# Optimization experiments

Measured on AMD Instinct MI355X. Metric: run time of the kernel, lower is better.

Reference implementation:

```python
import jax, jax.numpy as jnp
import numpy as np

N_FEAT = 64      # number of continuous features
N_BINS = 255     # bin edges per feature (EBM default) -> 256 score slots incl. OOV
N_PAIRS = 32     # interaction terms
BATCH = 262144


def _bin_indices(edges, x):
    """TF Discretization (searchsorted right) + IntegerLookup(vocab=range(B), OOV->0).
    edges: [N, B] sorted per row; x: [batch, N] -> int32 [batch, N] in [0, B]."""
    idx = jax.vmap(lambda e, col: jnp.searchsorted(e, col, side='right'),
                   in_axes=(0, 1), out_axes=1)(edges, x)  # [batch, N], values 0..B
    B = edges.shape[1]
    # IntegerLookup: value v in {0..B-1} -> v+1 ; value B (not in vocab) -> OOV index 0
    return jnp.where(idx < B, idx + 1, 0)


def setup_inputs() -> dict:
    key = jax.random.key(0)
    ks = jax.random.split(key, 6)
    x = jax.random.normal(ks[0], (BATCH, N_FEAT), dtype=jnp.float32)
    edges = jnp.sort(jax.random.normal(ks[1], (N_FEAT, N_BINS), dtype=jnp.float32), axis=1)
    pair_edges = jnp.sort(jax.random.normal(ks[2], (N_FEAT, N_BINS), dtype=jnp.float32), axis=1)
    w = jax.random.normal(ks[3], (N_FEAT, N_BINS + 1), dtype=jnp.float32) * 0.1
    tables = jax.random.normal(ks[4], (N_PAIRS, N_BINS + 1, N_BINS + 1), dtype=jnp.float32) * 0.1
    pairs = jax.random.randint(ks[5], (N_PAIRS, 2), 0, N_FEAT, dtype=jnp.int32)
    bias = jnp.zeros((1,), dtype=jnp.float32)
    return {"x": x, "edges": edges, "w": w, "pair_edges": pair_edges,
            "pairs": pairs, "tables": tables, "bias": bias}


def reference(x, edges, w, pair_edges, pairs, tables, bias):
    # --- per-feature main effects: one_hot(idx) @ Dense(1) == gather w[f, idx] ---
    idx = _bin_indices(edges, x)                                  # [batch, N]
    feat = w[jnp.arange(N_FEAT)[None, :], idx]                    # [batch, N]
    # --- pairwise interactions: gather_nd on [L, R] lookup tables ---
    pidx = _bin_indices(pair_edges, x)                            # [batch, N]
    li = pidx[:, pairs[:, 0]]                                     # [batch, P]
    ri = pidx[:, pairs[:, 1]]                                     # [batch, P]
    inter = tables[jnp.arange(N_PAIRS)[None, :], li, ri]          # [batch, P]
    # --- BiasLayer: reduce_sum(concat, axis=1) + bias, then sigmoid ---
    logits = jnp.sum(feat, axis=1) + jnp.sum(inter, axis=1) + bias[0]
    return jax.nn.sigmoid(logits)                                  # [batch]
```

## Files before the change

kernel.cpp:

```cpp
#include <hip/hip_runtime.h>
#include <hip/hip_fp16.h>

#define NBINS 255
#define NPAIRS 32
#define BIGF 3.0e38f


__global__ void ebm_prep(const float* __restrict__ edges,
                         const float* __restrict__ pair_edges,
                         const float* __restrict__ w,
                         float* __restrict__ ws) {
    int tid = blockIdx.x * blockDim.x + threadIdx.x;
    int f = tid >> 8, j = tid & 255;
    float* E  = ws;
    float* PE = ws + 16384;
    float* ME = ws + 32768;
    float* MP = ws + 36864;
    float* CU = ws + 40960;
    float* CP = ws + 41984;
    __half* W = (__half*)(ws + 43008);
    E[tid]  = (j < NBINS) ? edges[f * NBINS + j]      : BIGF;
    PE[tid] = (j < NBINS) ? pair_edges[f * NBINS + j] : BIGF;
    int src = (j < 255) ? j + 1 : 0;
    W[tid]  = __float2half(w[f * 256 + src]);
    if (j < 64) {
        int idx = 4 * j + 3;
        ME[f * 64 + j] = (idx < NBINS) ? edges[f * NBINS + idx]      : BIGF;
        MP[f * 64 + j] = (idx < NBINS) ? pair_edges[f * NBINS + idx] : BIGF;
    }
    if (j < 16) {
        CU[f * 16 + j] = (j < 15) ? edges[f * NBINS + 16 * j + 15]      : BIGF;
        CP[f * 16 + j] = (j < 15) ? pair_edges[f * NBINS + 16 * j + 15] : BIGF;
    }
}

__global__ void ebm_prep_tables(const float* __restrict__ tables,
                                unsigned short* __restrict__ o) {
    int i = blockIdx.x * blockDim.x + threadIdx.x;
    int b = i & 255, a = (i >> 8) & 255, p = i >> 16;
    int ra = (a < 255) ? a + 1 : 0;
    int rb = (b < 255) ? b + 1 : 0;
    o[i] = __half_as_ushort(__float2half(tables[(p << 16) + (ra << 8) + rb]));
}

__device__ __forceinline__ unsigned pick16(const unsigned* pw, int s) {
    unsigned v01 = (s & 1) ? pw[1]  : pw[0];
    unsigned v23 = (s & 1) ? pw[3]  : pw[2];
    unsigned v45 = (s & 1) ? pw[5]  : pw[4];
    unsigned v67 = (s & 1) ? pw[7]  : pw[6];
    unsigned v89 = (s & 1) ? pw[9]  : pw[8];
    unsigned vab = (s & 1) ? pw[11] : pw[10];
    unsigned vcd = (s & 1) ? pw[13] : pw[12];
    unsigned vef = (s & 1) ? pw[15] : pw[14];
    unsigned w0 = (s & 2) ? v23 : v01;
    unsigned w1 = (s & 2) ? v67 : v45;
    unsigned w2 = (s & 2) ? vab : v89;
    unsigned w3 = (s & 2) ? vef : vcd;
    unsigned u0 = (s & 4) ? w1 : w0;
    unsigned u1 = (s & 4) ? w3 : w2;
    return (s & 8) ? u1 : u0;
}

__global__ __launch_bounds__(1024) void ebm_main(
    const float* __restrict__ x,
    const int*   __restrict__ pairs,
    const float* __restrict__ tables_f32,
    const float* __restrict__ bias,
    const float* __restrict__ ws,
    const __half* __restrict__ T16,
    int useT16,
    float*       __restrict__ out) {

    __shared__ float  sE[16384];
    __shared__ float  sPE[16384];
    __shared__ float4 sME[1024];
    __shared__ float4 sMP[1024];

    int tid = threadIdx.x;
    {
        const float4* w4 = (const float4*)ws;
        float4* dE = (float4*)sE;
        float4* dP = (float4*)sPE;
        for (int i = tid; i < 4096; i += 1024) {
            dE[i] = w4[i];
            dP[i] = w4[4096 + i];
        }
        if (tid < 1024) {
            sME[tid] = w4[8192 + tid];
            sMP[tid] = w4[9216 + tid];
        }
    }
    const float*  CU = ws + 40960;
    const float*  CP = ws + 41984;
    const __half* Wg = (const __half*)(ws + 43008);
    float bias0 = bias[0];

    __syncthreads();

    int row = blockIdx.x * 1024 + tid;
    const float4* x4 = (const float4*)x + row * 16;
    const float4* sE4 = (const float4*)sE;
    const float4* sP4 = (const float4*)sPE;

    float acc = 0.f;
    unsigned pw[16];

    float4 xg = x4[0];
#pragma unroll
    for (int g = 0; g < 16; ++g) {
        float4 xnext = xg;
        if (g < 15) xnext = x4[g + 1];
        float xf[4] = {xg.x, xg.y, xg.z, xg.w};

        int t[4];
#pragma unroll
        for (int j = 0; j < 4; ++j) {
            const float* cu = CU + (4 * g + j) * 16;
            int tt = 0;
#pragma unroll
            for (int k = 0; k < 15; ++k) tt += (xf[j] >= cu[k]);
            t[j] = tt;
        }
        int t2[4];
#pragma unroll
        for (int j = 0; j < 4; ++j) {
            const float* cp = CP + (4 * g + j) * 16;
            int tt = 0;
#pragma unroll
            for (int k = 0; k < 15; ++k) tt += (xf[j] >= cp[k]);
            t2[j] = tt;
        }
        float4 mu[4], mp[4];
#pragma unroll
        for (int j = 0; j < 4; ++j) mu[j] = sME[(4 * g + j) * 16 + t[j]];
#pragma unroll
        for (int j = 0; j < 4; ++j) mp[j] = sMP[(4 * g + j) * 16 + t2[j]];
        int lo[4], lo2[4];
        float4 fu[4], fp[4];
#pragma unroll
        for (int j = 0; j < 4; ++j) {
            int m = (xf[j] >= mu[j].x) + (xf[j] >= mu[j].y) + (xf[j] >= mu[j].z);
            lo[j] = 4 * t[j] + m;
            fu[j] = sE4[(4 * g + j) * 64 + lo[j]];
        }
#pragma unroll
        for (int j = 0; j < 4; ++j) {
            int m = (xf[j] >= mp[j].x) + (xf[j] >= mp[j].y) + (xf[j] >= mp[j].z);
            lo2[j] = 4 * t2[j] + m;
            fp[j] = sP4[(4 * g + j) * 64 + lo2[j]];
        }
#pragma unroll
        for (int j = 0; j < 4; ++j) {
            int c = 4 * lo[j] + (xf[j] >= fu[j].x) + (xf[j] >= fu[j].y) +
                    (xf[j] >= fu[j].z) + (xf[j] >= fu[j].w);
            acc += __half2float(Wg[(4 * g + j) * 256 + c]);
        }
        unsigned pword = 0;
#pragma unroll
        for (int j = 0; j < 4; ++j) {
            int c2 = 4 * lo2[j] + (xf[j] >= fp[j].x) + (xf[j] >= fp[j].y) +
                     (xf[j] >= fp[j].z) + (xf[j] >= fp[j].w);
            pword |= (unsigned)c2 << (8 * j);
        }
        pw[g] = pword;
        xg = xnext;
    }

    if (useT16) {
#pragma unroll
        for (int p = 0; p < NPAIRS; ++p) {
            int a = pairs[2 * p], b = pairs[2 * p + 1];
            unsigned wa = pick16(pw, a >> 2);
            unsigned wb = pick16(pw, b >> 2);
            int li = (wa >> ((a & 3) * 8)) & 255;
            int ri = (wb >> ((b & 3) * 8)) & 255;
            acc += __half2float(T16[(p << 16) + (li << 8) + ri]);
        }
    } else {
#pragma unroll
        for (int p = 0; p < NPAIRS; ++p) {
            int a = pairs[2 * p], b = pairs[2 * p + 1];
            unsigned wa = pick16(pw, a >> 2);
            unsigned wb = pick16(pw, b >> 2);
            int li = (wa >> ((a & 3) * 8)) & 255;
            int ri = (wb >> ((b & 3) * 8)) & 255;
            int lb = (li < 255) ? li + 1 : 0;
            int rb = (ri < 255) ? ri + 1 : 0;
            acc += tables_f32[(p << 16) + (lb << 8) + rb];
        }
    }

    out[row] = 1.0f / (1.0f + __expf(-(acc + bias0)));
}

extern "C" void kernel_launch(void* const* d_in, const int* in_sizes, int n_in,
                              void* d_out, int out_size, void* d_ws, size_t ws_size,
                              hipStream_t stream) {
    const float* x          = (const float*)d_in[0];
    const float* edges      = (const float*)d_in[1];
    const float* w          = (const float*)d_in[2];
    const float* pair_edges = (const float*)d_in[3];
    const int*   pairs      = (const int*)d_in[4];
    const float* tables     = (const float*)d_in[5];
    const float* bias       = (const float*)d_in[6];
    float* out = (float*)d_out;
    float* ws  = (float*)d_ws;

    int useT16 = (ws_size >= (size_t)4399104) ? 1 : 0;
    __half* T16 = (__half*)((char*)d_ws + 204800);

    ebm_prep<<<64, 256, 0, stream>>>(edges, pair_edges, w, ws);
    if (useT16) {
        ebm_prep_tables<<<2048, 1024, 0, stream>>>(tables, (unsigned short*)T16);
    }
    ebm_main<<<256, 1024, 0, stream>>>(x, pairs, tables, bias, ws, T16, useT16, out);
}
```

Before: 193.5 us.

## Split each row across two wavefront halves and halve shared memory footprint

Each block now handles 512 rows with two threads per row. Each half bins 32 features and handles 16 of the pair lookups, with the bin codes exchanged through shared memory and the partial sums combined before the sigmoid. Pair-edge arrays are read from global memory instead of being staged in LDS, which cuts LDS per block roughly in half so more blocks can be resident, and the grid doubles. This costs extra barriers, an LDS exchange step, and uncached-in-LDS global reads for the pair edges.

```diff
diff --git a/kernel.cpp b/kernel.cpp
--- a/kernel.cpp
+++ b/kernel.cpp
@@ -61,7 +61,7 @@
     return (s & 8) ? u1 : u0;
 }
 
-__global__ __launch_bounds__(1024) void ebm_main(
+__global__ __launch_bounds__(1024, 8) void ebm_main(
     const float* __restrict__ x,
     const int*   __restrict__ pairs,
     const float* __restrict__ tables_f32,
@@ -72,50 +72,49 @@
     float*       __restrict__ out) {
 
     __shared__ float  sE[16384];
-    __shared__ float  sPE[16384];
     __shared__ float4 sME[1024];
-    __shared__ float4 sMP[1024];
 
     int tid = threadIdx.x;
     {
         const float4* w4 = (const float4*)ws;
         float4* dE = (float4*)sE;
-        float4* dP = (float4*)sPE;
-        for (int i = tid; i < 4096; i += 1024) {
-            dE[i] = w4[i];
-            dP[i] = w4[4096 + i];
-        }
-        if (tid < 1024) {
-            sME[tid] = w4[8192 + tid];
-            sMP[tid] = w4[9216 + tid];
-        }
-    }
-    const float*  CU = ws + 40960;
-    const float*  CP = ws + 41984;
-    const __half* Wg = (const __half*)(ws + 43008);
+        for (int i = tid; i < 4096; i += 1024) dE[i] = w4[i];
+        sME[tid] = w4[8192 + tid];
+    }
+    const float*  CU  = ws + 40960;
+    const float*  CP  = ws + 41984;
+    const __half* Wg  = (const __half*)(ws + 43008);
+    const float4* PE4 = (const float4*)(ws + 16384);
+    const float4* MP4 = (const float4*)(ws + 36864);
     float bias0 = bias[0];
 
     __syncthreads();
 
-    int row = blockIdx.x * 1024 + tid;
-    const float4* x4 = (const float4*)x + row * 16;
+    int wv   = tid >> 6;
+    int lane = tid & 63;
+    int half = wv >> 3;
+    int halfU = __builtin_amdgcn_readfirstlane(half);
+    int rowl = (wv & 7) * 64 + lane;
+    int row  = blockIdx.x * 512 + rowl;
+
+    const float4* x4  = (const float4*)x + row * 16 + halfU * 8;
     const float4* sE4 = (const float4*)sE;
-    const float4* sP4 = (const float4*)sPE;
 
     float acc = 0.f;
-    unsigned pw[16];
+    unsigned pw[8];
 
     float4 xg = x4[0];
 #pragma unroll
-    for (int g = 0; g < 16; ++g) {
+    for (int g = 0; g < 8; ++g) {
+        int fb = (halfU * 8 + g) * 4;
         float4 xnext = xg;
-        if (g < 15) xnext = x4[g + 1];
+        if (g < 7) xnext = x4[g + 1];
         float xf[4] = {xg.x, xg.y, xg.z, xg.w};
 
         int t[4];
 #pragma unroll
         for (int j = 0; j < 4; ++j) {
-            const float* cu = CU + (4 * g + j) * 16;
+            const float* cu = CU + (fb + j) * 16;
             int tt = 0;
 #pragma unroll
             for (int k = 0; k < 15; ++k) tt += (xf[j] >= cu[k]);
@@ -124,7 +123,7 @@
         int t2[4];
 #pragma unroll
         for (int j = 0; j < 4; ++j) {
-            const float* cp = CP + (4 * g + j) * 16;
+            const float* cp = CP + (fb + j) * 16;
             int tt = 0;
 #pragma unroll
             for (int k = 0; k < 15; ++k) tt += (xf[j] >= cp[k]);
@@ -132,28 +131,28 @@
         }
         float4 mu[4], mp[4];
 #pragma unroll
-        for (int j = 0; j < 4; ++j) mu[j] = sME[(4 * g + j) * 16 + t[j]];
-#pragma unroll
-        for (int j = 0; j < 4; ++j) mp[j] = sMP[(4 * g + j) * 16 + t2[j]];
+        for (int j = 0; j < 4; ++j) mu[j] = sME[(fb + j) * 16 + t[j]];
+#pragma unroll
+        for (int j = 0; j < 4; ++j) mp[j] = MP4[(fb + j) * 16 + t2[j]];
         int lo[4], lo2[4];
         float4 fu[4], fp[4];
 #pragma unroll
         for (int j = 0; j < 4; ++j) {
             int m = (xf[j] >= mu[j].x) + (xf[j] >= mu[j].y) + (xf[j] >= mu[j].z);
             lo[j] = 4 * t[j] + m;
-            fu[j] = sE4[(4 * g + j) * 64 + lo[j]];
+            fu[j] = sE4[(fb + j) * 64 + lo[j]];
         }
 #pragma unroll
         for (int j = 0; j < 4; ++j) {
             int m = (xf[j] >= mp[j].x) + (xf[j] >= mp[j].y) + (xf[j] >= mp[j].z);
             lo2[j] = 4 * t2[j] + m;
-            fp[j] = sP4[(4 * g + j) * 64 + lo2[j]];
+            fp[j] = PE4[(fb + j) * 64 + lo2[j]];
         }
 #pragma unroll
         for (int j = 0; j < 4; ++j) {
             int c = 4 * lo[j] + (xf[j] >= fu[j].x) + (xf[j] >= fu[j].y) +
                     (xf[j] >= fu[j].z) + (xf[j] >= fu[j].w);
-            acc += __half2float(Wg[(4 * g + j) * 256 + c]);
+            acc += __half2float(Wg[(fb + j) * 256 + c]);
         }
         unsigned pword = 0;
 #pragma unroll
@@ -166,22 +165,43 @@
         xg = xnext;
     }
 
+    unsigned* scr  = (unsigned*)sE;
+    float*    accS = (float*)sME;
+    __syncthreads();
+#pragma unroll
+    for (int i = 0; i < 8; ++i)
+        scr[(i * 2 + halfU) * 512 + rowl] = pw[i];
+    __syncthreads();
+    unsigned oth[8];
+#pragma unroll
+    for (int i = 0; i < 8; ++i)
+        oth[i] = scr[(i * 2 + (1 - halfU)) * 512 + rowl];
+    unsigned pwAll[16];
+#pragma unroll
+    for (int i = 0; i < 8; ++i) {
+        pwAll[i]     = halfU ? oth[i] : pw[i];
+        pwAll[8 + i] = halfU ? pw[i]  : oth[i];
+    }
+
+    int pbase = halfU * 16;
     if (useT16) {
 #pragma unroll
-        for (int p = 0; p < NPAIRS; ++p) {
+        for (int q = 0; q < 16; ++q) {
+            int p = pbase + q;
             int a = pairs[2 * p], b = pairs[2 * p + 1];
-            unsigned wa = pick16(pw, a >> 2);
-            unsigned wb = pick16(pw, b >> 2);
+            unsigned wa = pick16(pwAll, a >> 2);
+            unsigned wb = pick16(pwAll, b >> 2);
             int li = (wa >> ((a & 3) * 8)) & 255;
             int ri = (wb >> ((b & 3) * 8)) & 255;
             acc += __half2float(T16[(p << 16) + (li << 8) + ri]);
         }
     } else {
 #pragma unroll
-        for (int p = 0; p < NPAIRS; ++p) {
+        for (int q = 0; q < 16; ++q) {
+            int p = pbase + q;
             int a = pairs[2 * p], b = pairs[2 * p + 1];
-            unsigned wa = pick16(pw, a >> 2);
-            unsigned wb = pick16(pw, b >> 2);
+            unsigned wa = pick16(pwAll, a >> 2);
+            unsigned wb = pick16(pwAll, b >> 2);
             int li = (wa >> ((a & 3) * 8)) & 255;
             int ri = (wb >> ((b & 3) * 8)) & 255;
             int lb = (li < 255) ? li + 1 : 0;
@@ -190,7 +210,12 @@
         }
     }
 
-    out[row] = 1.0f / (1.0f + __expf(-(acc + bias0)));
+    accS[halfU * 512 + rowl] = acc;
+    __syncthreads();
+    if (halfU == 0) {
+        float tot = acc + accS[512 + rowl];
+        out[row] = 1.0f / (1.0f + __expf(-(tot + bias0)));
+    }
 }
 
 extern "C" void kernel_launch(void* const* d_in, const int* in_sizes, int n_in,
@@ -213,5 +238,5 @@
     if (useT16) {
         ebm_prep_tables<<<2048, 1024, 0, stream>>>(tables, (unsigned short*)T16);
     }
-    ebm_main<<<256, 1024, 0, stream>>>(x, pairs, tables, bias, ws, T16, useT16, out);
-}
+    ebm_main<<<512, 1024, 0, stream>>>(x, pairs, tables, bias, ws, T16, useT16, out);
+}
```

Result: slower. 207.0 us (+7.0%).

## Software-pipeline bin search across feature groups and index pair bytes via LDS

Applied to the files above, without the earlier changes.

Restructures the main loop so the coarse search and first-level LDS lookups for the next feature group run while the current group finishes, and the weight gathers are deferred one iteration. The register select tree (pick16) for pair indices is replaced by staging the packed bin bytes in reused shared memory and reading them with byte loads. Pair feature ids are broadcast from one wave register with readlane instead of scalar loads. This raises register pressure and adds a barrier plus LDS stores, and it sets a launch-bounds occupancy hint.

```diff
diff --git a/kernel.cpp b/kernel.cpp
--- a/kernel.cpp
+++ b/kernel.cpp
@@ -43,25 +43,7 @@
     o[i] = __half_as_ushort(__float2half(tables[(p << 16) + (ra << 8) + rb]));
 }
 
-__device__ __forceinline__ unsigned pick16(const unsigned* pw, int s) {
-    unsigned v01 = (s & 1) ? pw[1]  : pw[0];
-    unsigned v23 = (s & 1) ? pw[3]  : pw[2];
-    unsigned v45 = (s & 1) ? pw[5]  : pw[4];
-    unsigned v67 = (s & 1) ? pw[7]  : pw[6];
-    unsigned v89 = (s & 1) ? pw[9]  : pw[8];
-    unsigned vab = (s & 1) ? pw[11] : pw[10];
-    unsigned vcd = (s & 1) ? pw[13] : pw[12];
-    unsigned vef = (s & 1) ? pw[15] : pw[14];
-    unsigned w0 = (s & 2) ? v23 : v01;
-    unsigned w1 = (s & 2) ? v67 : v45;
-    unsigned w2 = (s & 2) ? vab : v89;
-    unsigned w3 = (s & 2) ? vef : vcd;
-    unsigned u0 = (s & 4) ? w1 : w0;
-    unsigned u1 = (s & 4) ? w3 : w2;
-    return (s & 8) ? u1 : u0;
-}
-
-__global__ __launch_bounds__(1024) void ebm_main(
+__global__ __launch_bounds__(1024, 4) void ebm_main(
     const float* __restrict__ x,
     const int*   __restrict__ pairs,
     const float* __restrict__ tables_f32,
@@ -77,6 +59,7 @@
     __shared__ float4 sMP[1024];
 
     int tid = threadIdx.x;
+    int myab = pairs[tid & 63];
     {
         const float4* w4 = (const float4*)ws;
         float4* dE = (float4*)sE;
@@ -85,10 +68,8 @@
             dE[i] = w4[i];
             dP[i] = w4[4096 + i];
         }
-        if (tid < 1024) {
-            sME[tid] = w4[8192 + tid];
-            sMP[tid] = w4[9216 + tid];
-        }
+        sME[tid] = w4[8192 + tid];
+        sMP[tid] = w4[9216 + tid];
     }
     const float*  CU = ws + 40960;
     const float*  CP = ws + 41984;
@@ -98,62 +79,94 @@
     __syncthreads();
 
     int row = blockIdx.x * 1024 + tid;
-    const float4* x4 = (const float4*)x + row * 16;
+    const float4* x4  = (const float4*)x + row * 16;
     const float4* sE4 = (const float4*)sE;
     const float4* sP4 = (const float4*)sPE;
 
     float acc = 0.f;
     unsigned pw[16];
 
-    float4 xg = x4[0];
+    float4 xa = x4[0];
+    float4 xb = x4[1];
+    float xf[4] = {xa.x, xa.y, xa.z, xa.w};
+    int t[4], t2[4];
+#pragma unroll
+    for (int j = 0; j < 4; ++j) {
+        const float* cu = CU + j * 16;
+        int tt = 0;
+#pragma unroll
+        for (int k = 0; k < 15; ++k) tt += (xf[j] >= cu[k]);
+        t[j] = tt;
+    }
+#pragma unroll
+    for (int j = 0; j < 4; ++j) {
+        const float* cp = CP + j * 16;
+        int tt = 0;
+#pragma unroll
+        for (int k = 0; k < 15; ++k) tt += (xf[j] >= cp[k]);
+        t2[j] = tt;
+    }
+    float4 mu[4], mp[4];
+#pragma unroll
+    for (int j = 0; j < 4; ++j) mu[j] = sME[j * 16 + t[j]];
+#pragma unroll
+    for (int j = 0; j < 4; ++j) mp[j] = sMP[j * 16 + t2[j]];
+
+    __half wraw[4];
+#pragma unroll
+    for (int j = 0; j < 4; ++j) wraw[j] = __float2half(0.f);
+
 #pragma unroll
     for (int g = 0; g < 16; ++g) {
-        float4 xnext = xg;
-        if (g < 15) xnext = x4[g + 1];
-        float xf[4] = {xg.x, xg.y, xg.z, xg.w};
-
-        int t[4];
-#pragma unroll
-        for (int j = 0; j < 4; ++j) {
-            const float* cu = CU + (4 * g + j) * 16;
-            int tt = 0;
-#pragma unroll
-            for (int k = 0; k < 15; ++k) tt += (xf[j] >= cu[k]);
-            t[j] = tt;
-        }
-        int t2[4];
-#pragma unroll
-        for (int j = 0; j < 4; ++j) {
-            const float* cp = CP + (4 * g + j) * 16;
-            int tt = 0;
-#pragma unroll
-            for (int k = 0; k < 15; ++k) tt += (xf[j] >= cp[k]);
-            t2[j] = tt;
-        }
-        float4 mu[4], mp[4];
-#pragma unroll
-        for (int j = 0; j < 4; ++j) mu[j] = sME[(4 * g + j) * 16 + t[j]];
-#pragma unroll
-        for (int j = 0; j < 4; ++j) mp[j] = sMP[(4 * g + j) * 16 + t2[j]];
+        int fb = 4 * g;
         int lo[4], lo2[4];
         float4 fu[4], fp[4];
 #pragma unroll
         for (int j = 0; j < 4; ++j) {
             int m = (xf[j] >= mu[j].x) + (xf[j] >= mu[j].y) + (xf[j] >= mu[j].z);
             lo[j] = 4 * t[j] + m;
-            fu[j] = sE4[(4 * g + j) * 64 + lo[j]];
+            fu[j] = sE4[(fb + j) * 64 + lo[j]];
         }
 #pragma unroll
         for (int j = 0; j < 4; ++j) {
             int m = (xf[j] >= mp[j].x) + (xf[j] >= mp[j].y) + (xf[j] >= mp[j].z);
             lo2[j] = 4 * t2[j] + m;
-            fp[j] = sP4[(4 * g + j) * 64 + lo2[j]];
-        }
+            fp[j] = sP4[(fb + j) * 64 + lo2[j]];
+        }
+        float xfn[4] = {xb.x, xb.y, xb.z, xb.w};
+        int tn[4] = {0, 0, 0, 0}, t2n[4] = {0, 0, 0, 0};
+        if (g < 15) {
+#pragma unroll
+            for (int j = 0; j < 4; ++j) {
+                const float* cu = CU + (fb + 4 + j) * 16;
+                int tt = 0;
+#pragma unroll
+                for (int k = 0; k < 15; ++k) tt += (xfn[j] >= cu[k]);
+                tn[j] = tt;
+            }
+#pragma unroll
+            for (int j = 0; j < 4; ++j) {
+                const float* cp = CP + (fb + 4 + j) * 16;
+                int tt = 0;
+#pragma unroll
+                for (int k = 0; k < 15; ++k) tt += (xfn[j] >= cp[k]);
+                t2n[j] = tt;
+            }
+        }
+        float4 mun[4], mpn[4];
+        if (g < 15) {
+#pragma unroll
+            for (int j = 0; j < 4; ++j) mun[j] = sME[(fb + 4 + j) * 16 + tn[j]];
+#pragma unroll
+            for (int j = 0; j < 4; ++j) mpn[j] = sMP[(fb + 4 + j) * 16 + t2n[j]];
+        }
+#pragma unroll
+        for (int j = 0; j < 4; ++j) acc += __half2float(wraw[j]);
 #pragma unroll
         for (int j = 0; j < 4; ++j) {
             int c = 4 * lo[j] + (xf[j] >= fu[j].x) + (xf[j] >= fu[j].y) +
                     (xf[j] >= fu[j].z) + (xf[j] >= fu[j].w);
-            acc += __half2float(Wg[(4 * g + j) * 256 + c]);
+            wraw[j] = Wg[(fb + j) * 256 + c];
         }
         unsigned pword = 0;
 #pragma unroll
@@ -163,27 +176,42 @@
             pword |= (unsigned)c2 << (8 * j);
         }
         pw[g] = pword;
-        xg = xnext;
-    }
+        if (g < 15) {
+#pragma unroll
+            for (int j = 0; j < 4; ++j) {
+                xf[j] = xfn[j]; t[j] = tn[j]; t2[j] = t2n[j];
+                mu[j] = mun[j]; mp[j] = mpn[j];
+            }
+            xa = xb;
+            if (g < 14) xb = x4[g + 2];
+        }
+    }
+#pragma unroll
+    for (int j = 0; j < 4; ++j) acc += __half2float(wraw[j]);
+
+    __syncthreads();
+    unsigned* scr = (unsigned*)sE;
+#pragma unroll
+    for (int i = 0; i < 16; ++i) scr[i * 1024 + tid] = pw[i];
+    const unsigned char* scrB = (const unsigned char*)sE;
+    int boff = tid * 4;
 
     if (useT16) {
 #pragma unroll
         for (int p = 0; p < NPAIRS; ++p) {
-            int a = pairs[2 * p], b = pairs[2 * p + 1];
-            unsigned wa = pick16(pw, a >> 2);
-            unsigned wb = pick16(pw, b >> 2);
-            int li = (wa >> ((a & 3) * 8)) & 255;
-            int ri = (wb >> ((b & 3) * 8)) & 255;
+            int a = __builtin_amdgcn_readlane(myab, 2 * p);
+            int b = __builtin_amdgcn_readlane(myab, 2 * p + 1);
+            int li = scrB[(a >> 2) * 4096 + boff + (a & 3)];
+            int ri = scrB[(b >> 2) * 4096 + boff + (b & 3)];
             acc += __half2float(T16[(p << 16) + (li << 8) + ri]);
         }
     } else {
 #pragma unroll
         for (int p = 0; p < NPAIRS; ++p) {
-            int a = pairs[2 * p], b = pairs[2 * p + 1];
-            unsigned wa = pick16(pw, a >> 2);
-            unsigned wb = pick16(pw, b >> 2);
-            int li = (wa >> ((a & 3) * 8)) & 255;
-            int ri = (wb >> ((b & 3) * 8)) & 255;
+            int a = __builtin_amdgcn_readlane(myab, 2 * p);
+            int b = __builtin_amdgcn_readlane(myab, 2 * p + 1);
+            int li = scrB[(a >> 2) * 4096 + boff + (a & 3)];
+            int ri = scrB[(b >> 2) * 4096 + boff + (b & 3)];
             int lb = (li < 255) ? li + 1 : 0;
             int rb = (ri < 255) ? ri + 1 : 0;
             acc += tables_f32[(p << 16) + (lb << 8) + rb];
```

After: 200.7 us. 3.7% more time.

## Split main kernel into half-feature binning and separate pair-lookup kernels

Applied to the files above, without the earlier changes.

Replaces the single fused kernel with two kernels when workspace is large enough. The first bins each row using two blocks per 1024 rows, each handling half of the features with half the shared-memory edge tables, and writes partial logits and packed pair bins to global memory. The second kernel reads those back, does the 32 table lookups and applies the sigmoid. The aim is more blocks and less shared memory per block for better occupancy, paid for with extra global traffic (about 16 words per row) and one more launch. It only takes effect if the harness workspace exceeds the new size threshold.

```diff
diff --git a/kernel.cpp b/kernel.cpp
--- a/kernel.cpp
+++ b/kernel.cpp
@@ -43,6 +43,151 @@
     o[i] = __half_as_ushort(__float2half(tables[(p << 16) + (ra << 8) + rb]));
 }
 
+__global__ __launch_bounds__(1024, 8) void ebm_bin(
+    const float* __restrict__ x,
+    const float* __restrict__ ws,
+    float*       __restrict__ plog,
+    unsigned*    __restrict__ pbins) {
+
+    __shared__ float  sE[8192];
+    __shared__ float  sPE[8192];
+    __shared__ float4 sME[512];
+    __shared__ float4 sMP[512];
+
+    int tid = threadIdx.x;
+    int h = blockIdx.x & 1;
+    int rowbase = (blockIdx.x >> 1) * 1024;
+    {
+        const float4* w4 = (const float4*)ws;
+        float4* dE = (float4*)sE;
+        float4* dP = (float4*)sPE;
+        for (int i = tid; i < 2048; i += 1024) {
+            dE[i] = w4[h * 2048 + i];
+            dP[i] = w4[4096 + h * 2048 + i];
+        }
+        if (tid < 512) {
+            sME[tid] = w4[8192 + h * 512 + tid];
+            sMP[tid] = w4[9216 + h * 512 + tid];
+        }
+    }
+    const float*  CU = ws + 40960 + h * 512;
+    const float*  CP = ws + 41984 + h * 512;
+    const __half* Wg = (const __half*)(ws + 43008);
+
+    __syncthreads();
+
+    int row = rowbase + tid;
+    const float4* x4  = (const float4*)x + row * 16 + h * 8;
+    const float4* sE4 = (const float4*)sE;
+    const float4* sP4 = (const float4*)sPE;
+
+    float acc = 0.f;
+
+    float4 xg = x4[0];
+#pragma unroll
+    for (int g = 0; g < 8; ++g) {
+        int fb = 4 * g;
+        float4 xnext = xg;
+        if (g < 7) xnext = x4[g + 1];
+        float xf[4] = {xg.x, xg.y, xg.z, xg.w};
+
+        int t[4];
+#pragma unroll
+        for (int j = 0; j < 4; ++j) {
+            const float* cu = CU + (fb + j) * 16;
+            int tt = 0;
+#pragma unroll
+            for (int k = 0; k < 15; ++k) tt += (xf[j] >= cu[k]);
+            t[j] = tt;
+        }
+        int t2[4];
+#pragma unroll
+        for (int j = 0; j < 4; ++j) {
+            const float* cp = CP + (fb + j) * 16;
+            int tt = 0;
+#pragma unroll
+            for (int k = 0; k < 15; ++k) tt += (xf[j] >= cp[k]);
+            t2[j] = tt;
+        }
+        float4 mu[4], mp[4];
+#pragma unroll
+        for (int j = 0; j < 4; ++j) mu[j] = sME[(fb + j) * 16 + t[j]];
+#pragma unroll
+        for (int j = 0; j < 4; ++j) mp[j] = sMP[(fb + j) * 16 + t2[j]];
+        int lo[4], lo2[4];
+        float4 fu[4], fp[4];
+#pragma unroll
+        for (int j = 0; j < 4; ++j) {
+            int m = (xf[j] >= mu[j].x) + (xf[j] >= mu[j].y) + (xf[j] >= mu[j].z);
+            lo[j] = 4 * t[j] + m;
+            fu[j] = sE4[(fb + j) * 64 + lo[j]];
+        }
+#pragma unroll
+        for (int j = 0; j < 4; ++j) {
+            int m = (xf[j] >= mp[j].x) + (xf[j] >= mp[j].y) + (xf[j] >= mp[j].z);
+            lo2[j] = 4 * t2[j] + m;
+            fp[j] = sP4[(fb + j) * 64 + lo2[j]];
+        }
+#pragma unroll
+        for (int j = 0; j < 4; ++j) {
+            int c = 4 * lo[j] + (xf[j] >= fu[j].x) + (xf[j] >= fu[j].y) +
+                    (xf[j] >= fu[j].z) + (xf[j] >= fu[j].w);
+            acc += __half2float(Wg[(h * 32 + fb + j) * 256 + c]);
+        }
+        unsigned pword = 0;
+#pragma unroll
+        for (int j = 0; j < 4; ++j) {
+            int c2 = 4 * lo2[j] + (xf[j] >= fp[j].x) + (xf[j] >= fp[j].y) +
+                     (xf[j] >= fp[j].z) + (xf[j] >= fp[j].w);
+            pword |= (unsigned)c2 << (8 * j);
+        }
+        pbins[(h * 8 + g) * 262144 + row] = pword;
+        xg = xnext;
+    }
+
+    plog[h * 262144 + row] = acc;
+}
+
+__global__ __launch_bounds__(1024, 8) void ebm_pairs(
+    const int*      __restrict__ pairs,
+    const float*    __restrict__ tables_f32,
+    const float*    __restrict__ bias,
+    const float*    __restrict__ plog,
+    const unsigned* __restrict__ pbins,
+    const __half*   __restrict__ T16,
+    int useT16,
+    float*          __restrict__ out) {
+
+    int row = blockIdx.x * 1024 + threadIdx.x;
+    float acc = plog[row] + plog[262144 + row] + bias[0];
+
+    if (useT16) {
+#pragma unroll
+        for (int p = 0; p < NPAIRS; ++p) {
+            int a = pairs[2 * p], b = pairs[2 * p + 1];
+            unsigned wa = pbins[(a >> 2) * 262144 + row];
+            unsigned wb = pbins[(b >> 2) * 262144 + row];
+            int li = (wa >> ((a & 3) * 8)) & 255;
+            int ri = (wb >> ((b & 3) * 8)) & 255;
+            acc += __half2float(T16[(p << 16) + (li << 8) + ri]);
+        }
+    } else {
+#pragma unroll
+        for (int p = 0; p < NPAIRS; ++p) {
+            int a = pairs[2 * p], b = pairs[2 * p + 1];
+            unsigned wa = pbins[(a >> 2) * 262144 + row];
+            unsigned wb = pbins[(b >> 2) * 262144 + row];
+            int li = (wa >> ((a & 3) * 8)) & 255;
+            int ri = (wb >> ((b & 3) * 8)) & 255;
+            int lb = (li < 255) ? li + 1 : 0;
+            int rb = (ri < 255) ? ri + 1 : 0;
+            acc += tables_f32[(p << 16) + (lb << 8) + rb];
+        }
+    }
+
+    out[row] = 1.0f / (1.0f + __expf(-acc));
+}
+
 __device__ __forceinline__ unsigned pick16(const unsigned* pw, int s) {
     unsigned v01 = (s & 1) ? pw[1]  : pw[0];
     unsigned v23 = (s & 1) ? pw[3]  : pw[2];
@@ -61,7 +206,7 @@
     return (s & 8) ? u1 : u0;
 }
 
-__global__ __launch_bounds__(1024) void ebm_main(
+__global__ __launch_bounds__(1024, 4) void ebm_main_mono(
     const float* __restrict__ x,
     const int*   __restrict__ pairs,
     const float* __restrict__ tables_f32,
@@ -85,10 +230,8 @@
             dE[i] = w4[i];
             dP[i] = w4[4096 + i];
         }
-        if (tid < 1024) {
-            sME[tid] = w4[8192 + tid];
-            sMP[tid] = w4[9216 + tid];
-        }
+        sME[tid] = w4[8192 + tid];
+        sMP[tid] = w4[9216 + tid];
     }
     const float*  CU = ws + 40960;
     const float*  CP = ws + 41984;
@@ -98,7 +241,7 @@
     __syncthreads();
 
     int row = blockIdx.x * 1024 + tid;
-    const float4* x4 = (const float4*)x + row * 16;
+    const float4* x4  = (const float4*)x + row * 16;
     const float4* sE4 = (const float4*)sE;
     const float4* sP4 = (const float4*)sPE;
 
@@ -108,6 +251,7 @@
     float4 xg = x4[0];
 #pragma unroll
     for (int g = 0; g < 16; ++g) {
+        int fb = 4 * g;
         float4 xnext = xg;
         if (g < 15) xnext = x4[g + 1];
         float xf[4] = {xg.x, xg.y, xg.z, xg.w};
@@ -115,7 +259,7 @@
         int t[4];
 #pragma unroll
         for (int j = 0; j < 4; ++j) {
-            const float* cu = CU + (4 * g + j) * 16;
+            const float* cu = CU + (fb + j) * 16;
             int tt = 0;
 #pragma unroll
             for (int k = 0; k < 15; ++k) tt += (xf[j] >= cu[k]);
@@ -124,7 +268,7 @@
         int t2[4];
 #pragma unroll
         for (int j = 0; j < 4; ++j) {
-            const float* cp = CP + (4 * g + j) * 16;
+            const float* cp = CP + (fb + j) * 16;
             int tt = 0;
 #pragma unroll
             for (int k = 0; k < 15; ++k) tt += (xf[j] >= cp[k]);
@@ -132,28 +276,28 @@
         }
         float4 mu[4], mp[4];
 #pragma unroll
-        for (int j = 0; j < 4; ++j) mu[j] = sME[(4 * g + j) * 16 + t[j]];
-#pragma unroll
-        for (int j = 0; j < 4; ++j) mp[j] = sMP[(4 * g + j) * 16 + t2[j]];
+        for (int j = 0; j < 4; ++j) mu[j] = sME[(fb + j) * 16 + t[j]];
+#pragma unroll
+        for (int j = 0; j < 4; ++j) mp[j] = sMP[(fb + j) * 16 + t2[j]];
         int lo[4], lo2[4];
         float4 fu[4], fp[4];
 #pragma unroll
         for (int j = 0; j < 4; ++j) {
             int m = (xf[j] >= mu[j].x) + (xf[j] >= mu[j].y) + (xf[j] >= mu[j].z);
             lo[j] = 4 * t[j] + m;
-            fu[j] = sE4[(4 * g + j) * 64 + lo[j]];
+            fu[j] = sE4[(fb + j) * 64 + lo[j]];
         }
 #pragma unroll
         for (int j = 0; j < 4; ++j) {
             int m = (xf[j] >= mp[j].x) + (xf[j] >= mp[j].y) + (xf[j] >= mp[j].z);
             lo2[j] = 4 * t2[j] + m;
-            fp[j] = sP4[(4 * g + j) * 64 + lo2[j]];
+            fp[j] = sP4[(fb + j) * 64 + lo2[j]];
         }
 #pragma unroll
         for (int j = 0; j < 4; ++j) {
             int c = 4 * lo[j] + (xf[j] >= fu[j].x) + (xf[j] >= fu[j].y) +
                     (xf[j] >= fu[j].z) + (xf[j] >= fu[j].w);
-            acc += __half2float(Wg[(4 * g + j) * 256 + c]);
+            acc += __half2float(Wg[(fb + j) * 256 + c]);
         }
         unsigned pword = 0;
 #pragma unroll
@@ -206,12 +350,22 @@
     float* out = (float*)d_out;
     float* ws  = (float*)d_ws;
 
-    int useT16 = (ws_size >= (size_t)4399104) ? 1 : 0;
-    __half* T16 = (__half*)((char*)d_ws + 204800);
+    int useT16  = (ws_size >= (size_t)4399104) ? 1 : 0;
+    int useSplit = (ws_size >= (size_t)23273472) ? 1 : 0;
+    __half*   T16   = (__half*)((char*)d_ws + 204800);
+    float*    plog  = (float*)((char*)d_ws + 4399104);
+    unsigned* pbins = (unsigned*)((char*)d_ws + 6496256);
 
     ebm_prep<<<64, 256, 0, stream>>>(edges, pair_edges, w, ws);
     if (useT16) {
         ebm_prep_tables<<<2048, 1024, 0, stream>>>(tables, (unsigned short*)T16);
     }
-    ebm_main<<<256, 1024, 0, stream>>>(x, pairs, tables, bias, ws, T16, useT16, out);
-}
+    if (useSplit) {
+        ebm_bin<<<512, 1024, 0, stream>>>(x, ws, plog, pbins);
+        ebm_pairs<<<256, 1024, 0, stream>>>(pairs, tables, bias, plog, pbins,
+                                            T16, useT16, out);
+    } else {
+        ebm_main_mono<<<256, 1024, 0, stream>>>(x, pairs, tables, bias, ws,
+                                                T16, useT16, out);
+    }
+}
```

Result: slower. 262.4 us (+35.6%).
